# Kernel tuning notes

Hardware: AMD Instinct MI355X
Metric: run time of the kernel (lower is better)

The kernel has to match this reference:

```python
import jax, jax.numpy as jnp
import numpy as np

N_RAYS = 16384
T = 4194304          # total ragged samples across all rays (avg 256/ray)
M_PAD = 512          # static pad width, >= max per-ray count
STEPSIZE = 3.0 * np.sqrt(3.0) / 1024.0  # (aabb extent)*sqrt(3)/render_n_samples


def setup_inputs() -> dict:
    key = jax.random.key(0)
    k1, k2, k3 = jax.random.split(key, 3)
    rays = jax.random.normal(k1, (N_RAYS, 6), dtype=jnp.float32)
    dirs = rays[:, 3:6]
    dirs = dirs / jnp.linalg.norm(dirs, axis=-1, keepdims=True)
    rays_chunk = jnp.concatenate([rays[:, 0:3], dirs], axis=-1)
    # ragged sample list from ray_marching: sorted ray ids -> ragged counts
    ray_indices = jnp.sort(jax.random.randint(k2, (T,), 0, N_RAYS, dtype=jnp.int32))
    t_starts = jax.random.uniform(k3, (T,), jnp.float32, 0.1, 5.0)
    t_ends = t_starts + jnp.float32(STEPSIZE)
    return {"rays_chunk": rays_chunk, "ray_indices": ray_indices,
            "t_starts": t_starts, "t_ends": t_ends, "max_samps": M_PAD}


def reference(rays_chunk, ray_indices, t_starts, t_ends, max_samps):
    N = rays_chunk.shape[0]
    Tn = ray_indices.shape[0]
    origins = rays_chunk[:, 0:3]
    viewdirs = rays_chunk[:, 3:6]

    pz_vals = (t_starts + t_ends) * 0.5              # [T]
    pdists = t_ends - t_starts                       # [T]
    xyz = origins[ray_indices] + pz_vals[:, None] * viewdirs[ray_indices]  # [T,3]
    # append 0 size channel -> (M, 4) premasked valid sample points
    xyz_sampled = jnp.concatenate([xyz, jnp.zeros((Tn, 1), xyz.dtype)], axis=-1)

    # per-ray counts (== torch.unique(..., return_counts=True) scattered to N)
    counts = jax.ops.segment_sum(jnp.ones((Tn,), jnp.int32), ray_indices,
                                 num_segments=N)                 # [N]
    offsets = jnp.cumsum(counts) - counts                        # exclusive cumsum
    pos = jnp.arange(Tn, dtype=jnp.int32) - offsets[ray_indices] # slot within ray

    ray_valid = jnp.arange(max_samps)[None, :] < counts[:, None] # [N, M] bool

    # boolean-mask scatters dists[ray_valid]=pdists etc., done as indexed scatter
    z_vals = jnp.zeros((N, max_samps), t_starts.dtype).at[ray_indices, pos].set(pz_vals)
    dists = jnp.zeros((N, max_samps), t_starts.dtype).at[ray_indices, pos].set(pdists)
    xyz_sampled_w = jnp.zeros((N, max_samps, 4), xyz.dtype).at[ray_indices, pos].set(xyz_sampled)

    whole_valid = jnp.ones((N,), dtype=bool)
    # original returns (xyzs, ray_valid, M, z_vals, dists, whole_valid);
    # M is the static pad width here; xyz_sampled_w appended to keep the
    # padded-scatter path (the kernel-headroom op) live.
    return (xyz_sampled, ray_valid, z_vals, dists, whole_valid, xyz_sampled_w)
```

## Files before the change

kernel.cpp:

```cpp
#include <hip/hip_runtime.h>

#define M_PAD 512

typedef float f32x4 __attribute__((ext_vector_type(4)));

__device__ __forceinline__ int lower_bound_seeded(const int* __restrict__ ri,
                                                  int T, int N, int target,
                                                  int lane) {
    int guess = (int)(((long long)target * T) / N);
    int W = 4096;
    int lo = max(0, guess - W), hi = min(T, guess + W);
    while (true) {
        bool okLo = (lo == 0) || (ri[lo - 1] < target);
        bool okHi = (hi == T) || (ri[hi] >= target);
        if (okLo && okHi) break;
        W <<= 3;
        lo = max(0, guess - W); hi = min(T, guess + W);
    }
    while (hi - lo > 64) {
        int len = hi - lo;
        int probe = lo + (len * (lane + 1)) / 65;
        int v = ri[probe];
        unsigned long long m = __ballot(v < target);
        int k = __popcll(m);
        int nlo = (k == 0)  ? lo : lo + (len * k) / 65;
        int nhi = (k == 64) ? hi : lo + (len * (k + 1)) / 65;
        lo = nlo; hi = nhi;
    }
    int p = lo + lane;
    int v = (p < hi) ? ri[p] : 2147483647;
    unsigned long long m = __ballot(v < target);
    return lo + __popcll(m);
}

__global__ __launch_bounds__(1024)
void mono_kernel(const float* __restrict__ rays,
                 const int* __restrict__ ri,
                 const float* __restrict__ ts,
                 const float* __restrict__ te,
                 float* __restrict__ xyz_out,
                 float* __restrict__ ray_valid,
                 float* __restrict__ z_vals,
                 float* __restrict__ dists,
                 float* __restrict__ xyz_w,
                 float* __restrict__ whole_valid,
                 int N, int T) {
    const int r0 = blockIdx.x * 2;
    const int tid = threadIdx.x;
    const int wave = tid >> 6, lane = tid & 63;

    __shared__ int sh[3];
    if (wave < 3) {
        int lb = lower_bound_seeded(ri, T, N, r0 + wave, lane);
        if (lane == 0) sh[wave] = lb;
    }
    __syncthreads();

    {
        const int k = tid >> 9;
        const int j = tid & (M_PAD - 1);
        const int r = r0 + k;
        const int s = sh[k];
        const int cnt = sh[k + 1] - s;

        f32x4 pt = {0.f, 0.f, 0.f, 0.f};
        if (j < cnt) {
            int i = s + j;
            float a = ts[i], bb = te[i];
            float z = (a + bb) * 0.5f;
            const float* rc = rays + (size_t)r * 6;
            pt.x = fmaf(z, rc[3], rc[0]);
            pt.y = fmaf(z, rc[4], rc[1]);
            pt.z = fmaf(z, rc[5], rc[2]);
            __builtin_nontemporal_store(pt, reinterpret_cast<f32x4*>(xyz_out) + i);
        }
        __builtin_nontemporal_store(pt,
            reinterpret_cast<f32x4*>(xyz_w) + ((size_t)r << 9) + j);

        if (j == 0) whole_valid[r] = 1.0f;
    }

    if (tid < 256) {
        const int q  = tid << 2;
        const int k  = q >> 9;
        const int j0 = q & (M_PAD - 1);
        const int r  = r0 + k;
        const int s  = sh[k];
        const int cnt = sh[k + 1] - s;

        f32x4 z4 = {0.f, 0.f, 0.f, 0.f};
        f32x4 d4 = {0.f, 0.f, 0.f, 0.f};
        f32x4 v4 = {0.f, 0.f, 0.f, 0.f};
        #pragma unroll
        for (int e = 0; e < 4; ++e) {
            int j = j0 + e;
            if (j < cnt) {
                int i = s + j;
                float a = ts[i], bb = te[i];
                z4[e] = (a + bb) * 0.5f;
                d4[e] = bb - a;
                v4[e] = 1.0f;
            }
        }
        size_t base4 = (((size_t)r << 9) + j0) >> 2;
        __builtin_nontemporal_store(z4, reinterpret_cast<f32x4*>(z_vals)    + base4);
        __builtin_nontemporal_store(d4, reinterpret_cast<f32x4*>(dists)     + base4);
        __builtin_nontemporal_store(v4, reinterpret_cast<f32x4*>(ray_valid) + base4);
    }
}

extern "C" void kernel_launch(void* const* d_in, const int* in_sizes, int n_in,
                              void* d_out, int out_size, void* d_ws, size_t ws_size,
                              hipStream_t stream) {
    const float* rays = (const float*)d_in[0];
    const int*   ri   = (const int*)d_in[1];
    const float* ts   = (const float*)d_in[2];
    const float* te   = (const float*)d_in[3];
    const int N = in_sizes[0] / 6;
    const int T = in_sizes[1];

    float* out         = (float*)d_out;
    float* xyz_out     = out;
    float* ray_valid   = xyz_out + (size_t)T * 4;
    float* z_vals      = ray_valid + (size_t)N * M_PAD;
    float* dists       = z_vals + (size_t)N * M_PAD;
    float* whole_valid = dists + (size_t)N * M_PAD;
    float* xyz_w       = whole_valid + N;

    mono_kernel<<<N / 2, 1024, 0, stream>>>(rays, ri, ts, te,
                                            xyz_out, ray_valid, z_vals,
                                            dists, xyz_w, whole_valid, N, T);
}
```

Measured before the change: 75.07 us.

## Split kernel into specialized 256-thread blocks for xyz and per-ray scalar outputs

```diff
diff --git a/kernel.cpp b/kernel.cpp
--- a/kernel.cpp
+++ b/kernel.cpp
@@ -33,7 +33,7 @@
     return lo + __popcll(m);
 }
 
-__global__ __launch_bounds__(1024)
+__global__ __launch_bounds__(256)
 void mono_kernel(const float* __restrict__ rays,
                  const int* __restrict__ ri,
                  const float* __restrict__ ts,
@@ -45,23 +45,21 @@
                  float* __restrict__ xyz_w,
                  float* __restrict__ whole_valid,
                  int N, int T) {
-    const int r0 = blockIdx.x * 2;
     const int tid = threadIdx.x;
     const int wave = tid >> 6, lane = tid & 63;
+    const int GW = N * 2;
+    __shared__ int sh[3];
 
-    __shared__ int sh[3];
-    if (wave < 3) {
-        int lb = lower_bound_seeded(ri, T, N, r0 + wave, lane);
-        if (lane == 0) sh[wave] = lb;
-    }
-    __syncthreads();
-
-    {
-        const int k = tid >> 9;
-        const int j = tid & (M_PAD - 1);
-        const int r = r0 + k;
-        const int s = sh[k];
-        const int cnt = sh[k + 1] - s;
+    if ((int)blockIdx.x < GW) {
+        const int b = blockIdx.x;
+        const int r = b >> 1, h = b & 1;
+        if (wave < 2) {
+            int lb = lower_bound_seeded(ri, T, N, r + wave, lane);
+            if (lane == 0) sh[wave] = lb;
+        }
+        __syncthreads();
+        const int s = sh[0], cnt = sh[1] - s;
+        const int j = h * 256 + tid;
 
         f32x4 pt = {0.f, 0.f, 0.f, 0.f};
         if (j < cnt) {
@@ -76,16 +74,19 @@
         }
         __builtin_nontemporal_store(pt,
             reinterpret_cast<f32x4*>(xyz_w) + ((size_t)r << 9) + j);
-
-        if (j == 0) whole_valid[r] = 1.0f;
-    }
-
-    if (tid < 256) {
-        const int q  = tid << 2;
-        const int k  = q >> 9;
-        const int j0 = q & (M_PAD - 1);
-        const int r  = r0 + k;
-        const int s  = sh[k];
+    } else {
+        const int b = blockIdx.x - GW;
+        const int r0 = b * 2;
+        if (wave < 3) {
+            int lb = lower_bound_seeded(ri, T, N, r0 + wave, lane);
+            if (lane == 0) sh[wave] = lb;
+        }
+        __syncthreads();
+        const int k = tid >> 7;
+        const int local = tid & 127;
+        const int j0 = local << 2;
+        const int r = r0 + k;
+        const int s = sh[k];
         const int cnt = sh[k + 1] - s;
 
         f32x4 z4 = {0.f, 0.f, 0.f, 0.f};
@@ -102,10 +103,13 @@
                 v4[e] = 1.0f;
             }
         }
-        size_t base4 = (((size_t)r << 9) + j0) >> 2;
+        size_t base4 = ((size_t)r << 7) + local;
         __builtin_nontemporal_store(z4, reinterpret_cast<f32x4*>(z_vals)    + base4);
         __builtin_nontemporal_store(d4, reinterpret_cast<f32x4*>(dists)     + base4);
         __builtin_nontemporal_store(v4, reinterpret_cast<f32x4*>(ray_valid) + base4);
+
+        if (tid == 0)   whole_valid[r0]     = 1.0f;
+        if (tid == 128) whole_valid[r0 + 1] = 1.0f;
     }
 }
 
@@ -127,7 +131,8 @@
     float* whole_valid = dists + (size_t)N * M_PAD;
     float* xyz_w       = whole_valid + N;
 
-    mono_kernel<<<N / 2, 1024, 0, stream>>>(rays, ri, ts, te,
-                                            xyz_out, ray_valid, z_vals,
-                                            dists, xyz_w, whole_valid, N, T);
+    const int grid = N * 2 + N / 2;
+    mono_kernel<<<grid, 256, 0, stream>>>(rays, ri, ts, te,
+                                          xyz_out, ray_valid, z_vals,
+                                          dists, xyz_w, whole_valid, N, T);
 }
```

Measured after the change: 93.12 us. 24.0% more time.
